# Kernel tuning notes

Hardware: AMD Instinct MI355X
Metric: run time of the kernel (lower is better)

Reference implementation:

```python
import jax, jax.numpy as jnp
import numpy as np

B, N, K, D, H, L, MAXF = 32, 4096, 1024, 1024, 16, 2, 4096


def _ln(x, g, b, eps=1e-5):
    m = jnp.mean(x, -1, keepdims=True)
    v = jnp.mean((x - m) ** 2, -1, keepdims=True)
    return (x - m) * jax.lax.rsqrt(v + eps) * g + b


def _mha(q, k, v, in_w, in_b, out_w, out_b):
    # torch nn.MultiheadAttention (batch_first) with packed in_proj
    Bq, Lq, Dm = q.shape
    Lk = k.shape[1]
    dh = Dm // H
    wq, wk, wv = jnp.split(in_w, 3, axis=0)
    bq, bk, bv = jnp.split(in_b, 3)
    qp = (q @ wq.T + bq).reshape(Bq, Lq, H, dh)
    kp = (k @ wk.T + bk).reshape(Bq, Lk, H, dh)
    vp = (v @ wv.T + bv).reshape(Bq, Lk, H, dh)
    s = jnp.einsum('bqhd,bkhd->bhqk', qp, kp) * (dh ** -0.5)
    a = jax.nn.softmax(s, axis=-1)
    o = jnp.einsum('bhqk,bkhd->bqhd', a, vp).reshape(Bq, Lq, Dm)
    return o @ out_w.T + out_b


def setup_inputs() -> dict:
    key = jax.random.key(0)
    ks = iter(jax.random.split(key, 64))
    p = lambda *s: 0.02 * jax.random.normal(next(ks), s, jnp.float32)
    inp = {
        'frame_tokens': jax.random.normal(next(ks), (B, N, D), jnp.float32),
        'kv_salient': jax.random.normal(next(ks), (B, K, D), jnp.float32),
        'max_init': jax.random.normal(next(ks), (B, D), jnp.float32),
        'query_base': p(1, 2, D),
        'role_w': p(2, D),
        'time_w': p(MAXF, D),
        'ln1_g': jnp.ones((L, D)), 'ln1_b': jnp.zeros((L, D)),
        'sa_in_w': p(L, 3 * D, D), 'sa_in_b': jnp.zeros((L, 3 * D)),
        'sa_out_w': p(L, D, D), 'sa_out_b': jnp.zeros((L, D)),
        'ln2_g': jnp.ones((L, D)), 'ln2_b': jnp.zeros((L, D)),
        'cg_in_w': p(L, 3 * D, D), 'cg_in_b': jnp.zeros((L, 3 * D)),
        'cg_out_w': p(L, D, D), 'cg_out_b': jnp.zeros((L, D)),
        'cs_in_w': p(L, 3 * D, D), 'cs_in_b': jnp.zeros((L, 3 * D)),
        'cs_out_w': p(L, D, D), 'cs_out_b': jnp.zeros((L, D)),
        'ln3_g': jnp.ones((L, D)), 'ln3_b': jnp.zeros((L, D)),
        'ffn_w1': p(L, 4 * D, D), 'ffn_b1': jnp.zeros((L, 4 * D)),
        'ffn_w2': p(L, D, 4 * D), 'ffn_b2': jnp.zeros((L, D)),
        'out_g': jnp.ones((D,)), 'out_b': jnp.zeros((D,)),
        'frame_idx': jax.random.randint(next(ks), (B,), 0, MAXF),
    }
    return inp


def reference(frame_tokens, kv_salient, max_init, query_base, role_w, time_w,
              ln1_g, ln1_b, sa_in_w, sa_in_b, sa_out_w, sa_out_b,
              ln2_g, ln2_b, cg_in_w, cg_in_b, cg_out_w, cg_out_b,
              cs_in_w, cs_in_b, cs_out_w, cs_out_b, ln3_g, ln3_b,
              ffn_w1, ffn_b1, ffn_w2, ffn_b2, out_g, out_b, frame_idx):
    # q init: [mean token, max-init token] + learned query + role + temporal embeds
    mean_tok = frame_tokens.mean(1)                      # (B, D)
    q = jnp.stack([mean_tok, max_init], axis=1)          # (B, 2, D)
    t_emb = time_w[jnp.clip(frame_idx, 0, MAXF - 1)]     # (B, D)
    q = q + query_base + role_w[None] + t_emb[:, None, :]
    for l in range(L):
        x = _ln(q, ln1_g[l], ln1_b[l])
        q = q + _mha(x, x, x, sa_in_w[l], sa_in_b[l], sa_out_w[l], sa_out_b[l])
        qn = _ln(q, ln2_g[l], ln2_b[l])
        qA = _mha(qn[:, :1], frame_tokens, frame_tokens,
                  cg_in_w[l], cg_in_b[l], cg_out_w[l], cg_out_b[l])
        qB = _mha(qn[:, 1:], kv_salient, kv_salient,
                  cs_in_w[l], cs_in_b[l], cs_out_w[l], cs_out_b[l])
        q = q + jnp.concatenate([qA, qB], axis=1)
        h = _ln(q, ln3_g[l], ln3_b[l])
        h = jax.nn.gelu(h @ ffn_w1[l].T + ffn_b1[l], approximate=False)
        q = q + h @ ffn_w2[l].T + ffn_b2[l]
    return _ln(q, out_g, out_b)                          # (B, 2, D)
```

## Files before the change

### kernel.cpp

```cpp
#include <hip/hip_runtime.h>

typedef unsigned short u16;
typedef __bf16 bf16x8 __attribute__((ext_vector_type(8)));
typedef float  f32x4  __attribute__((ext_vector_type(4)));

static constexpr int B = 32, N = 4096, KV = 1024, D = 1024, H = 16, MAXF = 4096;

__global__ __launch_bounds__(256) void mean_kernel(const float* __restrict__ x, float* __restrict__ macc){
  int b = blockIdx.x, ch = blockIdx.y;
  int d0 = threadIdx.x*4;
  const float* p = x + ((size_t)b*N + (size_t)ch*128)*D + d0;
  float a0=0.f,a1=0.f,a2=0.f,a3=0.f;
  for(int k=0;k<128;k++){
    float4 v = *(const float4*)(p + (size_t)k*D);
    a0 += v.x; a1 += v.y; a2 += v.z; a3 += v.w;
  }
  atomicAdd(&macc[b*D + d0 + 0], a0);
  atomicAdd(&macc[b*D + d0 + 1], a1);
  atomicAdd(&macc[b*D + d0 + 2], a2);
  atomicAdd(&macc[b*D + d0 + 3], a3);
}

__global__ __launch_bounds__(256) void convt_kernel(const float* __restrict__ x,
    u16* __restrict__ xb, u16* __restrict__ xt, float* __restrict__ macc, int Nk){
  int b  = blockIdx.z;
  int t0 = blockIdx.x*64, d0 = blockIdx.y*64;
  __shared__ u16 tile[64][70];
  __shared__ float rsum[16][64];
  int tid = threadIdx.x;
  int rr = tid>>4, c4 = (tid&15)*4;
  const float* src = x  + ((size_t)b*Nk + t0)*D + d0;
  u16*         xbp = xb + ((size_t)b*Nk + t0)*D + d0;
  float s0=0.f,s1=0.f,s2=0.f,s3=0.f;
  for(int it=0; it<4; it++){
    int r = rr + it*16;
    float4 v = *(const float4*)(src + (size_t)r*D + c4);
    s0+=v.x; s1+=v.y; s2+=v.z; s3+=v.w;
    __bf16 e0=(__bf16)v.x, e1=(__bf16)v.y, e2=(__bf16)v.z, e3=(__bf16)v.w;
    u16 u0=*(u16*)&e0, u1=*(u16*)&e1, u2=*(u16*)&e2, u3=*(u16*)&e3;
    tile[r][c4+0]=u0; tile[r][c4+1]=u1; tile[r][c4+2]=u2; tile[r][c4+3]=u3;
    ushort4 w4; w4.x=u0; w4.y=u1; w4.z=u2; w4.w=u3;
    *(ushort4*)(xbp + (size_t)r*D + c4) = w4;
  }
  if(macc){
    rsum[rr][c4+0]=s0; rsum[rr][c4+1]=s1; rsum[rr][c4+2]=s2; rsum[rr][c4+3]=s3;
  }
  __syncthreads();
  u16* xtp = xt + ((size_t)b*D + d0)*Nk + t0;
  for(int it=0; it<4; it++){
    int dr = rr + it*16;
    ushort4 w4;
    w4.x = tile[c4+0][dr]; w4.y = tile[c4+1][dr];
    w4.z = tile[c4+2][dr]; w4.w = tile[c4+3][dr];
    *(ushort4*)(xtp + (size_t)dr*Nk + c4) = w4;
  }
  if(macc && tid < 64){
    float s = 0.f;
    #pragma unroll
    for(int i2=0;i2<16;i2++) s += rsum[i2][tid];
    atomicAdd(&macc[(size_t)b*D + d0 + tid], s);
  }
}

__global__ __launch_bounds__(256) void qinit_kernel(const float* __restrict__ macc,
    const float* __restrict__ maxini, const float* __restrict__ qbase, const float* __restrict__ rolew,
    const float* __restrict__ timew, const int* __restrict__ fidx, float* __restrict__ q){
  int b = blockIdx.x;
  int fi = fidx[b]; fi = fi < 0 ? 0 : (fi > MAXF-1 ? MAXF-1 : fi);
  int d0 = threadIdx.x*4;
  float4 te = *(const float4*)(timew + (size_t)fi*D + d0);
  float4 q0 = *(const float4*)(qbase + d0);
  float4 q1 = *(const float4*)(qbase + D + d0);
  float4 r0 = *(const float4*)(rolew + d0);
  float4 r1 = *(const float4*)(rolew + D + d0);
  float4 mi = *(const float4*)(maxini + (size_t)b*D + d0);
  const float invN = 1.0f/(float)N;
  float* o0 = q + (size_t)(2*b)*D + d0;
  float* o1 = q + (size_t)(2*b+1)*D + d0;
  o0[0] = macc[b*D+d0+0]*invN + q0.x + r0.x + te.x;
  o0[1] = macc[b*D+d0+1]*invN + q0.y + r0.y + te.y;
  o0[2] = macc[b*D+d0+2]*invN + q0.z + r0.z + te.z;
  o0[3] = macc[b*D+d0+3]*invN + q0.w + r0.w + te.w;
  o1[0] = mi.x + q1.x + r1.x + te.x;
  o1[1] = mi.y + q1.y + r1.y + te.y;
  o1[2] = mi.z + q1.z + r1.z + te.z;
  o1[3] = mi.w + q1.w + r1.w + te.w;
}

__global__ __launch_bounds__(256) void ln_kernel(const float* __restrict__ in, float* __restrict__ outp,
    const float* __restrict__ g, const float* __restrict__ bb){
  int r = blockIdx.x;
  int d0 = threadIdx.x*4;
  float4 v = *(const float4*)(in + (size_t)r*D + d0);
  float s = v.x+v.y+v.z+v.w;
  float ss = v.x*v.x + v.y*v.y + v.z*v.z + v.w*v.w;
  #pragma unroll
  for(int o=1;o<64;o<<=1){ s += __shfl_xor(s,o); ss += __shfl_xor(ss,o); }
  __shared__ float as_[4], aq_[4];
  int w = threadIdx.x>>6;
  if((threadIdx.x&63)==0){ as_[w]=s; aq_[w]=ss; }
  __syncthreads();
  s = as_[0]+as_[1]+as_[2]+as_[3];
  ss = aq_[0]+aq_[1]+aq_[2]+aq_[3];
  float mean = s*(1.0f/D);
  float var = ss*(1.0f/D) - mean*mean;
  float rstd = rsqrtf(var + 1e-5f);
  float4 gv = *(const float4*)(g + d0);
  float4 bv = *(const float4*)(bb + d0);
  float4 ov;
  ov.x = (v.x-mean)*rstd*gv.x + bv.x;
  ov.y = (v.y-mean)*rstd*gv.y + bv.y;
  ov.z = (v.z-mean)*rstd*gv.z + bv.z;
  ov.w = (v.w-mean)*rstd*gv.w + bv.w;
  *(float4*)(outp + (size_t)r*D + d0) = ov;
}

__global__ __launch_bounds__(256) void gemm_skinny(const float* __restrict__ in,
    const float* __restrict__ W0, const float* __restrict__ W1,
    const float* __restrict__ b0_, const float* __restrict__ b1_,
    float* __restrict__ out, int K, int Dout, int mode){
  int t = blockIdx.y;
  int wv = threadIdx.x >> 6, lane = threadIdx.x & 63;
  int j0 = blockIdx.x*16 + wv*4;
  const float* W = t ? W1 : W0;
  const float* bias = t ? b1_ : b0_;
  for(int bg=0; bg<8; bg++){
    int r0 = bg*8 + t;
    float acc[4][4];
    #pragma unroll
    for(int i=0;i<4;i++)
      #pragma unroll
      for(int j=0;j<4;j++) acc[i][j]=0.f;
    for(int kb = lane*4; kb < K; kb += 256){
      float4 a[4];
      #pragma unroll
      for(int rr=0;rr<4;rr++) a[rr] = *(const float4*)(in + (size_t)(r0 + rr*2)*K + kb);
      #pragma unroll
      for(int c=0;c<4;c++){
        float4 w = *(const float4*)(W + (size_t)(j0+c)*K + kb);
        #pragma unroll
        for(int rr=0;rr<4;rr++)
          acc[rr][c] += a[rr].x*w.x + a[rr].y*w.y + a[rr].z*w.z + a[rr].w*w.w;
      }
    }
    #pragma unroll
    for(int rr=0;rr<4;rr++)
      #pragma unroll
      for(int c=0;c<4;c++){
        float v2 = acc[rr][c];
        #pragma unroll
        for(int o=1;o<64;o<<=1) v2 += __shfl_xor(v2,o);
        acc[rr][c]=v2;
      }
    if(lane==0){
      #pragma unroll
      for(int rr=0;rr<4;rr++){
        int r = r0 + rr*2;
        #pragma unroll
        for(int c=0;c<4;c++){
          float sum = acc[rr][c] + bias[j0+c];
          size_t oi = (size_t)r*Dout + j0 + c;
          if(mode==1) out[oi] += sum;
          else if(mode==2) out[oi] = 0.5f*sum*(1.0f + erff(sum*0.70710678118654752f));
          else out[oi] = sum;
        }
      }
    }
  }
}

__global__ __launch_bounds__(256) void sa_kernel(const float* __restrict__ qkv, float* __restrict__ o){
  int b = blockIdx.x;
  __shared__ float sh[2*3072];
  __shared__ float sS[16][2][2];
  __shared__ float sA[16][2][2];
  for(int idx=threadIdx.x; idx<2*3072; idx+=256)
    sh[idx] = qkv[(size_t)(2*b)*3072 + idx];
  __syncthreads();
  if(threadIdx.x < 64){
    int h = threadIdx.x>>2, t = (threadIdx.x>>1)&1, t2 = threadIdx.x&1;
    const float* qp_ = &sh[t*3072 + h*64];
    const float* kp_ = &sh[t2*3072 + 1024 + h*64];
    float s = 0.f;
    for(int d2=0; d2<64; d2++) s += qp_[d2]*kp_[d2];
    sS[h][t][t2] = s*0.125f;
  }
  __syncthreads();
  if(threadIdx.x < 32){
    int h = threadIdx.x>>1, t = threadIdx.x&1;
    float s0=sS[h][t][0], s1=sS[h][t][1];
    float mx = fmaxf(s0,s1);
    float e0=expf(s0-mx), e1=expf(s1-mx);
    float inv = 1.0f/(e0+e1);
    sA[h][t][0]=e0*inv; sA[h][t][1]=e1*inv;
  }
  __syncthreads();
  for(int idx=threadIdx.x; idx<2048; idx+=256){
    int t = idx>>10, c = idx&1023, h = c>>6;
    o[(size_t)(2*b+t)*D + c] = sA[h][t][0]*sh[2048+c] + sA[h][t][1]*sh[3072+2048+c];
  }
}

__global__ __launch_bounds__(256) void u_kernel(const float* __restrict__ qp,
    const float* __restrict__ Wcg, const float* __restrict__ Wcs, u16* __restrict__ u){
  int r = blockIdx.x; int t = r & 1; int h = blockIdx.y;
  const float* Wk = (t ? Wcs : Wcg) + (size_t)(D + h*64)*D;
  __shared__ float qs[64];
  if(threadIdx.x < 64) qs[threadIdx.x] = qp[(size_t)r*D + h*64 + threadIdx.x] * 0.125f;
  __syncthreads();
  int j0 = threadIdx.x*4;
  float a0=0.f,a1=0.f,a2=0.f,a3=0.f;
  for(int d=0; d<64; d++){
    float qd = qs[d];
    float4 w = *(const float4*)(Wk + (size_t)d*D + j0);
    a0 += qd*w.x; a1 += qd*w.y; a2 += qd*w.z; a3 += qd*w.w;
  }
  __bf16* up = (__bf16*)u + ((size_t)r*H + h)*D + j0;
  up[0]=(__bf16)a0; up[1]=(__bf16)a1; up[2]=(__bf16)a2; up[3]=(__bf16)a3;
}

template<int CH>
__global__ __launch_bounds__(256) void flash_kernel(const float* __restrict__ xsrc, int Nk,
    const u16* __restrict__ U, int t,
    float* __restrict__ pm, float* __restrict__ pl, float* __restrict__ py){
  constexpr int SS = CH + 4;
  constexpr int PS = CH + 8;
  __shared__ float S_s[16*SS];
  __shared__ __align__(16) u16 P_s[16*PS];
  int b = blockIdx.x, c = blockIdx.y;
  int tid = threadIdx.x, lane = tid&63, wv = tid>>6, quad = lane>>4, l15 = lane&15;
  const float* xb = xsrc + ((size_t)b*Nk + (size_t)c*CH)*D;
  const u16* ub = U + ((size_t)(2*b + t)*H)*D;
  for(int mt = wv; mt < CH/16; mt += 4){
    f32x4 acc = {0.f,0.f,0.f,0.f};
    const float* arow = xb + (size_t)(mt*16 + l15)*D + quad*8;
    const u16* ubase = ub + (size_t)l15*D + quad*8;
    #pragma unroll 4
    for(int kb=0; kb<D; kb+=32){
      float4 p0 = *(const float4*)(arow + kb);
      float4 p1 = *(const float4*)(arow + kb + 4);
      bf16x8 af;
      af[0]=(__bf16)p0.x; af[1]=(__bf16)p0.y; af[2]=(__bf16)p0.z; af[3]=(__bf16)p0.w;
      af[4]=(__bf16)p1.x; af[5]=(__bf16)p1.y; af[6]=(__bf16)p1.z; af[7]=(__bf16)p1.w;
      bf16x8 bfr = *(const bf16x8*)(ubase + kb);
      acc = __builtin_amdgcn_mfma_f32_16x16x32_bf16(af, bfr, acc, 0, 0, 0);
    }
    int tokb = mt*16 + quad*4;
    #pragma unroll
    for(int g2=0; g2<4; g2++) S_s[l15*SS + tokb + g2] = acc[g2];
  }
  __syncthreads();
  {
    int h = tid>>4, sub = tid&15;
    float mx = -1e30f;
    for(int k2=sub;k2<CH;k2+=16) mx = fmaxf(mx, S_s[h*SS+k2]);
    #pragma unroll
    for(int o2=1;o2<16;o2<<=1) mx = fmaxf(mx, __shfl_xor(mx,o2));
    float ls = 0.f;
    for(int k2=sub;k2<CH;k2+=16){
      float p = expf(S_s[h*SS+k2]-mx);
      ((__bf16*)P_s)[h*PS + k2] = (__bf16)p;
      ls += p;
    }
    #pragma unroll
    for(int o2=1;o2<16;o2<<=1) ls += __shfl_xor(ls,o2);
    if(sub==0){
      size_t pi = ((size_t)c*B + b)*H + h;
      pm[pi]=mx; pl[pi]=ls;
    }
  }
  __syncthreads();
  f32x4 acc[16];
  #pragma unroll
  for(int i=0;i<16;i++) acc[i] = (f32x4){0.f,0.f,0.f,0.f};
  int dbase = wv*256 + l15;
  for(int kb=0; kb<CH; kb+=32){
    bf16x8 af = *(const bf16x8*)(P_s + l15*PS + kb + quad*8);
    const float* col0 = xb + (size_t)(kb + quad*8)*D + dbase;
    #pragma unroll
    for(int nt=0; nt<16; nt++){
      bf16x8 bfr;
      #pragma unroll
      for(int j=0;j<8;j++) bfr[j] = (__bf16)col0[(size_t)j*D + nt*16];
      acc[nt] = __builtin_amdgcn_mfma_f32_16x16x32_bf16(af, bfr, acc[nt], 0, 0, 0);
    }
  }
  float* pyb = py + (((size_t)c*B + b)*H)*D;
  #pragma unroll
  for(int nt=0;nt<16;nt++){
    int d = wv*256 + nt*16 + l15;
    #pragma unroll
    for(int g2=0;g2<4;g2++){
      int h = quad*4+g2;
      pyb[(size_t)h*D + d] = acc[nt][g2];
    }
  }
}

template<int CH>
__global__ __launch_bounds__(256) void flash2_kernel(const u16* __restrict__ XB,
    const u16* __restrict__ XT, int Nk, const u16* __restrict__ U, int t,
    float* __restrict__ pm, float* __restrict__ pl, float* __restrict__ py){
  constexpr int SS = CH + 4;
  constexpr int PS = CH + 8;
  __shared__ float S_s[16*SS];
  __shared__ __align__(16) u16 P_s[16*PS];
  int b = blockIdx.x, c = blockIdx.y;
  int tid = threadIdx.x, lane = tid&63, wv = tid>>6, quad = lane>>4, l15 = lane&15;
  const u16* xbb = XB + ((size_t)b*Nk + (size_t)c*CH)*D;
  const u16* xtb = XT + (size_t)b*D*Nk + (size_t)c*CH;
  const u16* ub  = U + ((size_t)(2*b + t)*H)*D;
  for(int mt = wv; mt < CH/16; mt += 4){
    f32x4 acc = {0.f,0.f,0.f,0.f};
    const u16* arow  = xbb + (size_t)(mt*16 + l15)*D + quad*8;
    const u16* ubase = ub  + (size_t)l15*D + quad*8;
    #pragma unroll 8
    for(int kb=0; kb<D; kb+=32){
      bf16x8 af  = *(const bf16x8*)(arow + kb);
      bf16x8 bfr = *(const bf16x8*)(ubase + kb);
      acc = __builtin_amdgcn_mfma_f32_16x16x32_bf16(af, bfr, acc, 0, 0, 0);
    }
    int tokb = mt*16 + quad*4;
    #pragma unroll
    for(int g2=0; g2<4; g2++) S_s[l15*SS + tokb + g2] = acc[g2];
  }
  __syncthreads();
  {
    int h = tid>>4, sub = tid&15;
    float mx = -1e30f;
    for(int k2=sub;k2<CH;k2+=16) mx = fmaxf(mx, S_s[h*SS+k2]);
    #pragma unroll
    for(int o2=1;o2<16;o2<<=1) mx = fmaxf(mx, __shfl_xor(mx,o2));
    float ls = 0.f;
    for(int k2=sub;k2<CH;k2+=16){
      float p = expf(S_s[h*SS+k2]-mx);
      ((__bf16*)P_s)[h*PS + k2] = (__bf16)p;
      ls += p;
    }
    #pragma unroll
    for(int o2=1;o2<16;o2<<=1) ls += __shfl_xor(ls,o2);
    if(sub==0){
      size_t pi = ((size_t)c*B + b)*H + h;
      pm[pi]=mx; pl[pi]=ls;
    }
  }
  __syncthreads();
  f32x4 acc[16];
  #pragma unroll
  for(int i=0;i<16;i++) acc[i] = (f32x4){0.f,0.f,0.f,0.f};
  const u16* xtw = xtb + (size_t)(wv*256 + l15)*Nk;
  for(int kb=0; kb<CH; kb+=32){
    bf16x8 af = *(const bf16x8*)(P_s + l15*PS + kb + quad*8);
    #pragma unroll
    for(int nt=0; nt<16; nt++){
      bf16x8 bfr = *(const bf16x8*)(xtw + (size_t)(nt*16)*Nk + kb + quad*8);
      acc[nt] = __builtin_amdgcn_mfma_f32_16x16x32_bf16(af, bfr, acc[nt], 0, 0, 0);
    }
  }
  float* pyb = py + (((size_t)c*B + b)*H)*D;
  #pragma unroll
  for(int nt=0;nt<16;nt++){
    int d = wv*256 + nt*16 + l15;
    #pragma unroll
    for(int g2=0;g2<4;g2++){
      int h = quad*4+g2;
      pyb[(size_t)h*D + d] = acc[nt][g2];
    }
  }
}

__global__ __launch_bounds__(256) void combine_kernel(const float* __restrict__ pm, const float* __restrict__ pl,
    const float* __restrict__ py, float* __restrict__ y, int t, int C){
  int b = blockIdx.x, h = blockIdx.y, tid = threadIdx.x;
  float mx = -1e30f;
  for(int c2=0;c2<C;c2++) mx = fmaxf(mx, pm[((size_t)c2*B+b)*H + h]);
  __shared__ float wsh[16];
  if(tid < C) wsh[tid] = expf(pm[((size_t)tid*B+b)*H + h] - mx);
  __syncthreads();
  float L = 0.f;
  for(int c2=0;c2<C;c2++) L += wsh[c2]*pl[((size_t)c2*B+b)*H + h];
  float inv = 1.0f/L;
  for(int d = tid; d < D; d += 256){
    float a = 0.f;
    for(int c2=0;c2<C;c2++) a += wsh[c2]*py[(((size_t)c2*B+b)*H + h)*D + d];
    y[((size_t)(2*b+t)*H + h)*D + d] = a*inv;
  }
}

__global__ __launch_bounds__(256) void headv_kernel(const float* __restrict__ y,
    const float* __restrict__ Wcg, const float* __restrict__ Wcs,
    const float* __restrict__ bcg, const float* __restrict__ bcs,
    float* __restrict__ o){
  int r = blockIdx.x, t = r&1, h = blockIdx.y;
  const float* Wv = (t?Wcs:Wcg) + (size_t)(2*D + h*64)*D;
  const float* bv = (t?bcs:bcg) + 2*D + h*64;
  __shared__ float ys[1024];
  int tid = threadIdx.x;
  *(float4*)&ys[tid*4] = *(const float4*)(y + ((size_t)r*H + h)*D + tid*4);
  __syncthreads();
  int wv2 = tid>>6, lane = tid&63;
  for(int dp = wv2; dp < 64; dp += 4){
    float a = 0.f;
    for(int jb = lane*4; jb < 1024; jb += 256){
      float4 w = *(const float4*)(Wv + (size_t)dp*D + jb);
      float4 yv = *(const float4*)&ys[jb];
      a += yv.x*w.x + yv.y*w.y + yv.z*w.z + yv.w*w.w;
    }
    #pragma unroll
    for(int o2=1;o2<64;o2<<=1) a += __shfl_xor(a,o2);
    if(lane==0) o[(size_t)r*D + h*64 + dp] = a + bv[dp];
  }
}

extern "C" void kernel_launch(void* const* d_in, const int* in_sizes, int n_in,
                              void* d_out, int out_size, void* d_ws, size_t ws_size,
                              hipStream_t stream){
  const float* frame  = (const float*)d_in[0];
  const float* sal    = (const float*)d_in[1];
  const float* maxini = (const float*)d_in[2];
  const float* qbase  = (const float*)d_in[3];
  const float* rolew  = (const float*)d_in[4];
  const float* timew  = (const float*)d_in[5];
  const float* ln1g   = (const float*)d_in[6];
  const float* ln1b   = (const float*)d_in[7];
  const float* sainw  = (const float*)d_in[8];
  const float* sainb  = (const float*)d_in[9];
  const float* saoutw = (const float*)d_in[10];
  const float* saoutb = (const float*)d_in[11];
  const float* ln2g   = (const float*)d_in[12];
  const float* ln2b   = (const float*)d_in[13];
  const float* cginw  = (const float*)d_in[14];
  const float* cginb  = (const float*)d_in[15];
  const float* cgoutw = (const float*)d_in[16];
  const float* cgoutb = (const float*)d_in[17];
  const float* csinw  = (const float*)d_in[18];
  const float* csinb  = (const float*)d_in[19];
  const float* csoutw = (const float*)d_in[20];
  const float* csoutb = (const float*)d_in[21];
  const float* ln3g   = (const float*)d_in[22];
  const float* ln3b   = (const float*)d_in[23];
  const float* ffnw1  = (const float*)d_in[24];
  const float* ffnb1  = (const float*)d_in[25];
  const float* ffnw2  = (const float*)d_in[26];
  const float* ffnb2  = (const float*)d_in[27];
  const float* outg   = (const float*)d_in[28];
  const float* outbb  = (const float*)d_in[29];
  const int* fidx     = (const int*)d_in[30];
  float* out = (float*)d_out;

  float* wsf = (float*)d_ws;
  float* MEAN = wsf + 0;
  float* Q    = wsf + 32768;
  float* X    = wsf + 98304;
  float* QKV  = wsf + 163840;
  float* O    = wsf + 360448;
  float* QP   = wsf + 425984;
  u16*   U    = (u16*)(wsf + 491520);
  float* Y    = wsf + 1015808;
  float* HH   = wsf + 2064384;
  float* PM   = wsf + 2326528;
  float* PL   = wsf + 2334720;
  float* PY   = wsf + 2342912;
  u16*   XBF  = (u16*)(wsf + 10731520);
  u16*   XTF  = XBF + (size_t)B*N*D;
  u16*   XBS  = XTF + (size_t)B*N*D;
  u16*   XTS  = XBS + (size_t)B*KV*D;
  const bool fastF = ws_size >= 579796992ull;
  const bool fastS = ws_size >= 714014720ull;

  hipMemsetAsync(MEAN, 0, (size_t)B*D*sizeof(float), stream);
  if(fastF){
    convt_kernel<<<dim3(N/64, D/64, B), 256, 0, stream>>>(frame, XBF, XTF, MEAN, N);
  }else{
    mean_kernel<<<dim3(B,32), 256, 0, stream>>>(frame, MEAN);
  }
  if(fastS){
    convt_kernel<<<dim3(KV/64, D/64, B), 256, 0, stream>>>(sal, XBS, XTS, nullptr, KV);
  }
  qinit_kernel<<<B, 256, 0, stream>>>(MEAN, maxini, qbase, rolew, timew, fidx, Q);

  for(int l=0; l<2; l++){
    size_t w3 = (size_t)l*3*D*D, w1 = (size_t)l*D*D, w4 = (size_t)l*4*D*D;
    size_t b3 = (size_t)l*3*D,   b1 = (size_t)l*D,   b4 = (size_t)l*4*D;

    ln_kernel<<<64,256,0,stream>>>(Q, X, ln1g+b1, ln1b+b1);
    gemm_skinny<<<dim3(3*D/16,2),256,0,stream>>>(X, sainw+w3, sainw+w3, sainb+b3, sainb+b3, QKV, D, 3*D, 0);
    sa_kernel<<<B,256,0,stream>>>(QKV, O);
    gemm_skinny<<<dim3(D/16,2),256,0,stream>>>(O, saoutw+w1, saoutw+w1, saoutb+b1, saoutb+b1, Q, D, D, 1);

    ln_kernel<<<64,256,0,stream>>>(Q, X, ln2g+b1, ln2b+b1);
    gemm_skinny<<<dim3(D/16,2),256,0,stream>>>(X, cginw+w3, csinw+w3, cginb+b3, csinb+b3, QP, D, D, 0);
    u_kernel<<<dim3(64,H),256,0,stream>>>(QP, cginw+w3, csinw+w3, U);

    if(fastF){
      flash2_kernel<256><<<dim3(B,16),256,0,stream>>>(XBF, XTF, N, U, 0, PM, PL, PY);
      combine_kernel<<<dim3(B,H),256,0,stream>>>(PM, PL, PY, Y, 0, 16);
    }else{
      flash_kernel<512><<<dim3(B,8),256,0,stream>>>(frame, N, U, 0, PM, PL, PY);
      combine_kernel<<<dim3(B,H),256,0,stream>>>(PM, PL, PY, Y, 0, 8);
    }
    if(fastS){
      flash2_kernel<64><<<dim3(B,16),256,0,stream>>>(XBS, XTS, KV, U, 1, PM, PL, PY);
      combine_kernel<<<dim3(B,H),256,0,stream>>>(PM, PL, PY, Y, 1, 16);
    }else{
      flash_kernel<128><<<dim3(B,8),256,0,stream>>>(sal, KV, U, 1, PM, PL, PY);
      combine_kernel<<<dim3(B,H),256,0,stream>>>(PM, PL, PY, Y, 1, 8);
    }

    headv_kernel<<<dim3(64,H),256,0,stream>>>(Y, cginw+w3, csinw+w3, cginb+b3, csinb+b3, O);
    gemm_skinny<<<dim3(D/16,2),256,0,stream>>>(O, cgoutw+w1, csoutw+w1, cgoutb+b1, csoutb+b1, Q, D, D, 1);

    ln_kernel<<<64,256,0,stream>>>(Q, X, ln3g+b1, ln3b+b1);
    gemm_skinny<<<dim3(4*D/16,2),256,0,stream>>>(X, ffnw1+w4, ffnw1+w4, ffnb1+b4, ffnb1+b4, HH, D, 4*D, 2);
    gemm_skinny<<<dim3(D/16,2),256,0,stream>>>(HH, ffnw2+w4, ffnw2+w4, ffnb2+b1, ffnb2+b1, Q, 4*D, D, 1);
  }
  ln_kernel<<<64,256,0,stream>>>(Q, out, outg, outbb);
}
```

Measured before the change: 2.358 ms.

## Use 8-wave flash blocks, larger salient chunks and a merged combine kernel

The flash attention kernel now runs 512 threads (8 waves). Each wave handles half as many output columns in the P·V stage, and 32 lanes per head do the softmax reduction. The salient stream now uses 128-token chunks over 8 blocks instead of 64-token chunks over 16, and writes its partials to separate buffers. That lets one combine kernel merge both streams in a single launch instead of two. The cost is a larger workspace requirement: if the workspace falls below the raised threshold, the salient path drops back to the slow fp32 flash kernel.

New measurement: 2.293 ms. 1.03x faster.

```diff
diff --git a/kernel.cpp b/kernel.cpp
--- a/kernel.cpp
+++ b/kernel.cpp
@@ -298,7 +298,7 @@
 }
 
 template<int CH>
-__global__ __launch_bounds__(256) void flash2_kernel(const u16* __restrict__ XB,
+__global__ __launch_bounds__(512) void flash3_kernel(const u16* __restrict__ XB,
     const u16* __restrict__ XT, int Nk, const u16* __restrict__ U, int t,
     float* __restrict__ pm, float* __restrict__ pl, float* __restrict__ py){
   constexpr int SS = CH + 4;
@@ -310,7 +310,7 @@
   const u16* xbb = XB + ((size_t)b*Nk + (size_t)c*CH)*D;
   const u16* xtb = XT + (size_t)b*D*Nk + (size_t)c*CH;
   const u16* ub  = U + ((size_t)(2*b + t)*H)*D;
-  for(int mt = wv; mt < CH/16; mt += 4){
+  for(int mt = wv; mt < CH/16; mt += 8){
     f32x4 acc = {0.f,0.f,0.f,0.f};
     const u16* arow  = xbb + (size_t)(mt*16 + l15)*D + quad*8;
     const u16* ubase = ub  + (size_t)l15*D + quad*8;
@@ -326,41 +326,41 @@
   }
   __syncthreads();
   {
-    int h = tid>>4, sub = tid&15;
+    int h = tid>>5, sub = tid&31;
     float mx = -1e30f;
-    for(int k2=sub;k2<CH;k2+=16) mx = fmaxf(mx, S_s[h*SS+k2]);
-    #pragma unroll
-    for(int o2=1;o2<16;o2<<=1) mx = fmaxf(mx, __shfl_xor(mx,o2));
+    for(int k2=sub;k2<CH;k2+=32) mx = fmaxf(mx, S_s[h*SS+k2]);
+    #pragma unroll
+    for(int o2=1;o2<32;o2<<=1) mx = fmaxf(mx, __shfl_xor(mx,o2));
     float ls = 0.f;
-    for(int k2=sub;k2<CH;k2+=16){
+    for(int k2=sub;k2<CH;k2+=32){
       float p = expf(S_s[h*SS+k2]-mx);
       ((__bf16*)P_s)[h*PS + k2] = (__bf16)p;
       ls += p;
     }
     #pragma unroll
-    for(int o2=1;o2<16;o2<<=1) ls += __shfl_xor(ls,o2);
+    for(int o2=1;o2<32;o2<<=1) ls += __shfl_xor(ls,o2);
     if(sub==0){
       size_t pi = ((size_t)c*B + b)*H + h;
       pm[pi]=mx; pl[pi]=ls;
     }
   }
   __syncthreads();
-  f32x4 acc[16];
+  f32x4 acc[8];
   #pragma unroll
-  for(int i=0;i<16;i++) acc[i] = (f32x4){0.f,0.f,0.f,0.f};
-  const u16* xtw = xtb + (size_t)(wv*256 + l15)*Nk;
+  for(int i=0;i<8;i++) acc[i] = (f32x4){0.f,0.f,0.f,0.f};
+  const u16* xtw = xtb + (size_t)(wv*128 + l15)*Nk;
   for(int kb=0; kb<CH; kb+=32){
     bf16x8 af = *(const bf16x8*)(P_s + l15*PS + kb + quad*8);
     #pragma unroll
-    for(int nt=0; nt<16; nt++){
+    for(int nt=0; nt<8; nt++){
       bf16x8 bfr = *(const bf16x8*)(xtw + (size_t)(nt*16)*Nk + kb + quad*8);
       acc[nt] = __builtin_amdgcn_mfma_f32_16x16x32_bf16(af, bfr, acc[nt], 0, 0, 0);
     }
   }
   float* pyb = py + (((size_t)c*B + b)*H)*D;
   #pragma unroll
-  for(int nt=0;nt<16;nt++){
-    int d = wv*256 + nt*16 + l15;
+  for(int nt=0;nt<8;nt++){
+    int d = wv*128 + nt*16 + l15;
     #pragma unroll
     for(int g2=0;g2<4;g2++){
       int h = quad*4+g2;
@@ -372,6 +372,30 @@
 __global__ __launch_bounds__(256) void combine_kernel(const float* __restrict__ pm, const float* __restrict__ pl,
     const float* __restrict__ py, float* __restrict__ y, int t, int C){
   int b = blockIdx.x, h = blockIdx.y, tid = threadIdx.x;
+  float mx = -1e30f;
+  for(int c2=0;c2<C;c2++) mx = fmaxf(mx, pm[((size_t)c2*B+b)*H + h]);
+  __shared__ float wsh[16];
+  if(tid < C) wsh[tid] = expf(pm[((size_t)tid*B+b)*H + h] - mx);
+  __syncthreads();
+  float L = 0.f;
+  for(int c2=0;c2<C;c2++) L += wsh[c2]*pl[((size_t)c2*B+b)*H + h];
+  float inv = 1.0f/L;
+  for(int d = tid; d < D; d += 256){
+    float a = 0.f;
+    for(int c2=0;c2<C;c2++) a += wsh[c2]*py[(((size_t)c2*B+b)*H + h)*D + d];
+    y[((size_t)(2*b+t)*H + h)*D + d] = a*inv;
+  }
+}
+
+__global__ __launch_bounds__(256) void combine2_kernel(
+    const float* __restrict__ pm0, const float* __restrict__ pl0, const float* __restrict__ py0,
+    const float* __restrict__ pm1, const float* __restrict__ pl1, const float* __restrict__ py1,
+    float* __restrict__ y){
+  int b = blockIdx.x, h = blockIdx.y, t = blockIdx.z, tid = threadIdx.x;
+  const float* pm = t ? pm1 : pm0;
+  const float* pl = t ? pl1 : pl0;
+  const float* py = t ? py1 : py0;
+  int C = t ? 8 : 16;
   float mx = -1e30f;
   for(int c2=0;c2<C;c2++) mx = fmaxf(mx, pm[((size_t)c2*B+b)*H + h]);
   __shared__ float wsh[16];
@@ -465,8 +489,11 @@
   u16*   XTF  = XBF + (size_t)B*N*D;
   u16*   XBS  = XTF + (size_t)B*N*D;
   u16*   XTS  = XBS + (size_t)B*KV*D;
+  float* PM2  = wsf + 178503680;
+  float* PL2  = wsf + 178507776;
+  float* PY2  = wsf + 178511872;
   const bool fastF = ws_size >= 579796992ull;
-  const bool fastS = ws_size >= 714014720ull;
+  const bool fastS = ws_size >= 730824704ull;
 
   hipMemsetAsync(MEAN, 0, (size_t)B*D*sizeof(float), stream);
   if(fastF){
@@ -492,17 +519,18 @@
     gemm_skinny<<<dim3(D/16,2),256,0,stream>>>(X, cginw+w3, csinw+w3, cginb+b3, csinb+b3, QP, D, D, 0);
     u_kernel<<<dim3(64,H),256,0,stream>>>(QP, cginw+w3, csinw+w3, U);
 
-    if(fastF){
-      flash2_kernel<256><<<dim3(B,16),256,0,stream>>>(XBF, XTF, N, U, 0, PM, PL, PY);
+    if(fastS){
+      flash3_kernel<256><<<dim3(B,16),512,0,stream>>>(XBF, XTF, N, U, 0, PM, PL, PY);
+      flash3_kernel<128><<<dim3(B,8),512,0,stream>>>(XBS, XTS, KV, U, 1, PM2, PL2, PY2);
+      combine2_kernel<<<dim3(B,H,2),256,0,stream>>>(PM, PL, PY, PM2, PL2, PY2, Y);
+    }else if(fastF){
+      flash3_kernel<256><<<dim3(B,16),512,0,stream>>>(XBF, XTF, N, U, 0, PM, PL, PY);
       combine_kernel<<<dim3(B,H),256,0,stream>>>(PM, PL, PY, Y, 0, 16);
+      flash_kernel<128><<<dim3(B,8),256,0,stream>>>(sal, KV, U, 1, PM, PL, PY);
+      combine_kernel<<<dim3(B,H),256,0,stream>>>(PM, PL, PY, Y, 1, 8);
     }else{
       flash_kernel<512><<<dim3(B,8),256,0,stream>>>(frame, N, U, 0, PM, PL, PY);
       combine_kernel<<<dim3(B,H),256,0,stream>>>(PM, PL, PY, Y, 0, 8);
-    }
-    if(fastS){
-      flash2_kernel<64><<<dim3(B,16),256,0,stream>>>(XBS, XTS, KV, U, 1, PM, PL, PY);
-      combine_kernel<<<dim3(B,H),256,0,stream>>>(PM, PL, PY, Y, 1, 16);
-    }else{
       flash_kernel<128><<<dim3(B,8),256,0,stream>>>(sal, KV, U, 1, PM, PL, PY);
       combine_kernel<<<dim3(B,H),256,0,stream>>>(PM, PL, PY, Y, 1, 8);
     }
```
